# Kernel tuning notes

Hardware: AMD Instinct MI355X
Metric: run time of the kernel (lower is better)

## Reference

```python
import jax, jax.numpy as jnp
import numpy as np

B, S, C = 16, 720, 862      # batch, seq_len, enc_in
P = 24                      # highest_freq_period
PAD = 720                   # seq_len % P == 0 -> pad_len == seq_len (no padding branch taken)
LQ = PAD // P               # 30, per-branch subsequence length == conv channels
DM = 128                    # d_model (PECBlock hidden conv channels)
EL = 2                      # e_layers
PRED = 336                  # pred_len
EPS = 1e-5                  # RevIN eps


def setup_inputs() -> dict:
    key = jax.random.key(0)
    ks = jax.random.split(key, 6)
    x = jax.random.normal(ks[0], (B, S, C), jnp.float32)
    # per-layer, per-branch pointwise conv weights (kernel_size=1, no bias)
    W1 = jax.random.normal(ks[1], (EL, P, DM, LQ), jnp.float32) * 0.05   # conv1: LQ -> DM
    W2 = jax.random.normal(ks[2], (EL, P, LQ, DM), jnp.float32) * 0.05   # conv2: DM -> LQ
    proj_w = jax.random.normal(ks[3], (PRED, S), jnp.float32) * 0.02      # Linear(seq_len, pred_len)
    proj_b = jnp.zeros((PRED,), jnp.float32)
    rev_w = jnp.ones((C,), jnp.float32)    # RevIN affine weight
    rev_b = jnp.zeros((C,), jnp.float32)   # RevIN affine bias
    return dict(x=x, W1=W1, W2=W2, proj_w=proj_w, proj_b=proj_b, rev_w=rev_w, rev_b=rev_b)


def reference(x, W1, W2, proj_w, proj_b, rev_w, rev_b):
    # RevIN 'norm': stats over time dim (unbiased=False var), affine
    mean = jnp.mean(x, axis=1, keepdims=True)
    stdev = jnp.sqrt(jnp.var(x, axis=1, keepdims=True) + EPS)
    xn = (x - mean) / stdev * rev_w + rev_b

    # seq_len % P == 0 so pad_time_series is identity
    x_padded = xn
    # NOTE: original loop feeds x_padded into EVERY block (not chained),
    # so each iteration overwrites y; replicated faithfully.
    # Strided gather idx::P == reshape (B,C,LQ,P) and index last axis;
    # scatter reassembly y[:,:,idx::P]=... == reshape back from (B,C,LQ,P).
    xs = x_padded.transpose(0, 2, 1).reshape(B, C, LQ, P)  # (B,C,LQ,P)
    y = x_padded
    for l in range(EL):
        h = jax.nn.gelu(jnp.einsum('pdq,bcqp->pbdc', W1[l], xs), approximate=False)  # (P,B,DM,C)
        ys = jnp.einsum('pqd,pbdc->bcqp', W2[l], h)                                  # (B,C,LQ,P)
        y = ys.reshape(B, C, PAD).transpose(0, 2, 1)                                 # (B,PAD,C)

    # PredictedProjection: Linear over time dim
    out = jnp.einsum('ps,bsc->bpc', proj_w, y[:, :S, :]) + proj_b[None, :, None]  # (B,PRED,C)

    # RevIN 'denorm'
    out = (out - rev_b) / (rev_w + EPS * EPS)
    out = out * stdev + mean
    return out
```

## Files before the change

### kernel.cpp

```cpp
#include <hip/hip_runtime.h>
#include <math.h>

typedef __attribute__((ext_vector_type(8))) short bf16x8;
typedef __attribute__((ext_vector_type(4))) short short4v;
typedef __attribute__((ext_vector_type(4))) float f32x4;

#define NB 16
#define NS 720
#define NC 862
#define NP 24
#define NQ 30
#define NDM 128
#define NPRED 336
#define BC (NB*NC)
#define SCH 10
#define SLEN 72
#define KP 768
#define PBASE (4*BC)
#define WOFF_F (24*BC)
#define NCOL (NB*NC)

__device__ __forceinline__ short f2bf(float f) {
    union { float f; unsigned u; } v; v.f = f;
    unsigned r = v.u + 0x7FFFu + ((v.u >> 16) & 1u);
    return (short)(r >> 16);
}

__device__ __forceinline__ float gelu_f(float h) {
    float hc = fminf(fmaxf(h, -8.f), 8.f);
    float z2 = hc * hc;
    float zz = hc * (0.79788456f + 0.035677408f * z2);
    float e  = __expf(-2.f * zz);
    return h * __builtin_amdgcn_rcpf(1.f + e);
}

__device__ __forceinline__ void gl_lds16(const void* g, void* l) {
    __builtin_amdgcn_global_load_lds(
        (const __attribute__((address_space(1))) unsigned int*)g,
        (__attribute__((address_space(3))) unsigned int*)l, 16, 0, 0);
}

__global__ __launch_bounds__(256) void stats_partial_k(const float* __restrict__ x,
                                                       float* __restrict__ ws) {
    int b = blockIdx.x, half = blockIdx.y, ch = blockIdx.z;
    int t = half * 256 + threadIdx.x;
    if (t >= NC / 2) return;
    const float2* xp = (const float2*)(x + ((size_t)b * NS + (size_t)ch * SLEN) * NC) + t;
    float2 s = {0.f, 0.f}, sq = {0.f, 0.f};
    #pragma unroll 4
    for (int i = 0; i < SLEN; ++i) {
        float2 v = xp[(size_t)i * (NC / 2)];
        s.x += v.x; s.y += v.y;
        sq.x += v.x * v.x; sq.y += v.y * v.y;
    }
    int idx = b * NC + t * 2;
    float* ps = ws + PBASE;
    *(float2*)&ps[(size_t)ch * BC + idx] = s;
    *(float2*)&ps[(size_t)(SCH + ch) * BC + idx] = sq;
}

__global__ __launch_bounds__(256) void stats_final_k(float* __restrict__ ws,
                                                     const float* __restrict__ revw,
                                                     const float* __restrict__ revb) {
    int idx = blockIdx.x * 256 + threadIdx.x;
    if (idx >= BC) return;
    const float* ps = ws + PBASE;
    float s = 0.f, sq = 0.f;
    #pragma unroll
    for (int ch = 0; ch < SCH; ++ch) {
        s  += ps[(size_t)ch * BC + idx];
        sq += ps[(size_t)(SCH + ch) * BC + idx];
    }
    int c = idx % NC;
    float mean  = s * (1.f / NS);
    float var   = sq * (1.f / NS) - mean * mean;
    float stdev = sqrtf(var + 1e-5f);
    float rstd  = 1.f / stdev;
    float aw = revw[c] * rstd;
    float u  = stdev / (revw[c] + 1e-10f);
    ws[idx]          = aw;
    ws[BC + idx]     = revb[c] - mean * aw;
    ws[2 * BC + idx] = u;
    ws[3 * BC + idx] = mean - revb[c] * u;
}

__global__ __launch_bounds__(256) void wprep_k(const float* __restrict__ W1,
                                               const float* __restrict__ W2,
                                               unsigned short* __restrict__ W1FF,
                                               unsigned short* __restrict__ W2FF) {
    int p = blockIdx.x, tid = threadIdx.x;
    const float* w1 = W1 + (size_t)(NP + p) * NDM * NQ;
    const float* w2 = W2 + (size_t)(NP + p) * NQ * NDM;
    #pragma unroll
    for (int pass = 0; pass < 2; ++pass) {
        int s = pass * 256 + tid;
        int l = s & 63, lr = l & 15, lg = l >> 4;
        {
            int dt = s >> 6;
            int d = dt * 16 + lr;
            bf16x8 v;
            #pragma unroll
            for (int j = 0; j < 8; ++j) {
                int q = 8 * lg + j;
                v[j] = f2bf(q < NQ ? w1[d * NQ + q] : 0.f);
            }
            ((bf16x8*)(W1FF + (size_t)p * 4096))[s] = v;
        }
        {
            int g = s >> 6, mi = g >> 2, ks = g & 3;
            int q = mi * 16 + lr, k = ks * 32 + 8 * lg;
            bf16x8 v;
            #pragma unroll
            for (int j = 0; j < 8; ++j)
                v[j] = f2bf(q < NQ ? w2[q * NDM + k + j] : 0.f);
            ((bf16x8*)(W2FF + (size_t)p * 4096))[s] = v;
        }
    }
}

__global__ __launch_bounds__(256) void pwprep_k(const float* __restrict__ pw,
                                                unsigned short* __restrict__ PWPF) {
    int t = blockIdx.x * 256 + threadIdx.x;
    if (t >= 24 * 24 * 64) return;
    int l = t & 63, ks = (t >> 6) % 24, st = t / (24 * 64);
    int lr = l & 15, lg = l >> 4;
    int m = st * 16 + lr;
    bf16x8 v;
    #pragma unroll
    for (int j = 0; j < 8; ++j) {
        int q = 8 * lg + j;
        v[j] = f2bf((m < NPRED && q < NQ) ? pw[(size_t)m * NS + q * NP + ks] : 0.f);
    }
    ((bf16x8*)PWPF)[t] = v;
}

__global__ __launch_bounds__(256) void branch_k(const float* __restrict__ x,
        const unsigned short* __restrict__ W1FF, const unsigned short* __restrict__ W2FF,
        const float* __restrict__ ws, unsigned short* __restrict__ y_t) {
    __shared__ __align__(16) short XsB[4 * 64 * 8];
    __shared__ __align__(16) short HB [16 * 64 * 8];
    int tid = threadIdx.x;
    int c0 = blockIdx.x * 64;
    int p  = blockIdx.y;
    int b  = blockIdx.z;

    {
        int c  = tid & 63, kb = tid >> 6;
        int cg = c0 + c;
        bool cv = cg < NC;
        int ce = cv ? cg : NC - 1;
        float aw = ws[b * NC + ce];
        float bw = ws[BC + b * NC + ce];
        const float* xb = x + ((size_t)b * NS + p) * NC + ce;
        bf16x8 v;
        #pragma unroll
        for (int j = 0; j < 8; ++j) {
            int q = kb * 8 + j;
            float val = (q < NQ && cv) ? xb[(size_t)q * NP * NC] * aw + bw : 0.f;
            v[j] = f2bf(val);
        }
        *(bf16x8*)&XsB[(size_t)(kb * 64 + (c ^ kb)) * 8] = v;
    }

    int w = tid >> 6, l = tid & 63, lr = l & 15, lg = l >> 4;
    f32x4 zf = {0.f, 0.f, 0.f, 0.f};
    const bf16x8* w1p = (const bf16x8*)(W1FF + (size_t)p * 4096);
    const bf16x8* w2p = (const bf16x8*)(W2FF + (size_t)p * 4096);
    bf16x8 a0 = w1p[(2 * w) * 64 + l];
    bf16x8 a1 = w1p[(2 * w + 1) * 64 + l];

    __syncthreads();

    f32x4 hc[2][4];
    #pragma unroll
    for (int ni = 0; ni < 4; ++ni) {
        bf16x8 bfr = *(const bf16x8*)&XsB[(size_t)(lg * 64 + ((ni * 16 + lr) ^ lg)) * 8];
        hc[0][ni] = __builtin_amdgcn_mfma_f32_16x16x32_bf16(a0, bfr, zf, 0, 0, 0);
        hc[1][ni] = __builtin_amdgcn_mfma_f32_16x16x32_bf16(a1, bfr, zf, 0, 0, 0);
    }
    #pragma unroll
    for (int mi2 = 0; mi2 < 2; ++mi2) {
        int d0 = (2 * w + mi2) * 16 + 4 * lg;
        int kb = d0 >> 3, sub = d0 & 7;
        #pragma unroll
        for (int ni = 0; ni < 4; ++ni) {
            short4v v;
            #pragma unroll
            for (int r = 0; r < 4; ++r)
                v[r] = f2bf(gelu_f(hc[mi2][ni][r]));
            int col = ni * 16 + lr;
            *(short4v*)&HB[(size_t)(kb * 64 + (col ^ kb)) * 8 + sub] = v;
        }
    }
    __syncthreads();

    f32x4 yacc[2] = {zf, zf};
    #pragma unroll
    for (int ks = 0; ks < 4; ++ks) {
        int kb = ks * 4 + lg;
        bf16x8 hfr = *(const bf16x8*)&HB[(size_t)(kb * 64 + ((w * 16 + lr) ^ kb)) * 8];
        #pragma unroll
        for (int mi = 0; mi < 2; ++mi) {
            bf16x8 w2f = w2p[(mi * 4 + ks) * 64 + l];
            yacc[mi] = __builtin_amdgcn_mfma_f32_16x16x32_bf16(w2f, hfr, yacc[mi], 0, 0, 0);
        }
    }
    int cg2 = c0 + w * 16 + lr;
    if (cg2 < NC) {
        unsigned short* base = y_t + ((size_t)(b * NC + cg2)) * KP + p * 32;
        #pragma unroll
        for (int mi = 0; mi < 2; ++mi) {
            int q0 = mi * 16 + 4 * lg;
            short4v v;
            #pragma unroll
            for (int r = 0; r < 4; ++r)
                v[r] = (q0 + r < NQ) ? f2bf(yacc[mi][r]) : (short)0;
            *(short4v*)(base + q0) = v;
        }
    }
}

__global__ __launch_bounds__(256, 3) void proj_k(const unsigned short* __restrict__ PWPF,
        const float* __restrict__ pb, const float* __restrict__ ws,
        const unsigned short* __restrict__ y_t, float* __restrict__ out) {
    __shared__ __align__(16) short L[2][16 * 512];
    int tid = threadIdx.x;
    int w = tid >> 6, l = tid & 63, lr = l & 15, lg = l >> 4;
    int wm = w >> 1, wn = w & 1;
    int n0 = blockIdx.x * 128, m0 = blockIdx.y * 128;
    f32x4 zf = {0.f, 0.f, 0.f, 0.f};
    f32x4 acc[4][4];
    #pragma unroll
    for (int mi = 0; mi < 4; ++mi)
        #pragma unroll
        for (int nj = 0; nj < 4; ++nj) acc[mi][nj] = zf;

    int cB0 = n0 + w * 16 + lr;        if (cB0 > NCOL - 1) cB0 = NCOL - 1;
    int cB1 = n0 + (w + 4) * 16 + lr;  if (cB1 > NCOL - 1) cB1 = NCOL - 1;
    const unsigned short* sA0 = PWPF + ((size_t)(m0 / 16 + w) * 24) * 512 + (size_t)l * 8;
    const unsigned short* sA1 = PWPF + ((size_t)(m0 / 16 + w + 4) * 24) * 512 + (size_t)l * 8;
    const unsigned short* sB0 = y_t + (size_t)cB0 * KP + lg * 8;
    const unsigned short* sB1 = y_t + (size_t)cB1 * KP + lg * 8;

#define STAGE(BUF, KS) do {                                          \
        gl_lds16(sA0 + (size_t)(KS) * 512, &L[BUF][(w) * 512]);      \
        gl_lds16(sA1 + (size_t)(KS) * 512, &L[BUF][(w + 4) * 512]);  \
        gl_lds16(sB0 + (size_t)(KS) * 32,  &L[BUF][(8 + w) * 512]);  \
        gl_lds16(sB1 + (size_t)(KS) * 32,  &L[BUF][(12 + w) * 512]); \
    } while (0)

    STAGE(0, 0);
    __syncthreads();
    int cur = 0;
    for (int ks = 0; ks < 24; ++ks) {
        if (ks + 1 < 24) STAGE(cur ^ 1, ks + 1);
        const short* Lc = L[cur];
        bf16x8 bfr[4];
        #pragma unroll
        for (int nj = 0; nj < 4; ++nj)
            bfr[nj] = *(const bf16x8*)&Lc[(8 + wn * 4 + nj) * 512 + l * 8];
        #pragma unroll
        for (int mi = 0; mi < 4; ++mi) {
            bf16x8 a = *(const bf16x8*)&Lc[(wm * 4 + mi) * 512 + l * 8];
            #pragma unroll
            for (int nj = 0; nj < 4; ++nj)
                acc[mi][nj] = __builtin_amdgcn_mfma_f32_16x16x32_bf16(a, bfr[nj], acc[mi][nj], 0, 0, 0);
        }
        __syncthreads();
        cur ^= 1;
    }
#undef STAGE

    #pragma unroll
    for (int mi = 0; mi < 4; ++mi) {
        #pragma unroll
        for (int r = 0; r < 4; ++r) {
            int pr = m0 + wm * 64 + mi * 16 + 4 * lg + r;
            if (pr >= NPRED) continue;
            float bias = pb[pr];
            #pragma unroll
            for (int nj = 0; nj < 4; ++nj) {
                int cg = n0 + (wn * 4 + nj) * 16 + lr;
                if (cg >= NCOL) continue;
                int bb = cg / NC;
                int cc = cg - bb * NC;
                out[((size_t)bb * NPRED + pr) * NC + cc] =
                    (acc[mi][nj][r] + bias) * ws[2 * BC + cg] + ws[3 * BC + cg];
            }
        }
    }
}

extern "C" void kernel_launch(void* const* d_in, const int* in_sizes, int n_in,
                              void* d_out, int out_size, void* d_ws, size_t ws_size,
                              hipStream_t stream) {
    const float* x   = (const float*)d_in[0];
    const float* W1  = (const float*)d_in[1];
    const float* W2  = (const float*)d_in[2];
    const float* pw  = (const float*)d_in[3];
    const float* pb  = (const float*)d_in[4];
    const float* rw  = (const float*)d_in[5];
    const float* rb  = (const float*)d_in[6];
    float* out = (float*)d_out;
    float* ws  = (float*)d_ws;
    unsigned short* W1FF = (unsigned short*)(ws + WOFF_F);
    unsigned short* W2FF = W1FF + NP * 4096;
    unsigned short* PWPF = W2FF + NP * 4096;
    unsigned short* y_t  = PWPF + 24 * 24 * 64 * 8;

    stats_partial_k<<<dim3(NB, 2, SCH), 256, 0, stream>>>(x, ws);
    wprep_k<<<dim3(NP), 256, 0, stream>>>(W1, W2, W1FF, W2FF);
    pwprep_k<<<dim3((24 * 24 * 64 + 255) / 256), 256, 0, stream>>>(pw, PWPF);
    stats_final_k<<<dim3((BC + 255) / 256), 256, 0, stream>>>(ws, rw, rb);
    branch_k<<<dim3(14, NP, NB), 256, 0, stream>>>(x, W1FF, W2FF, ws, y_t);
    proj_k<<<dim3((NCOL + 127) / 128, 3), 256, 0, stream>>>(PWPF, pb, ws, y_t, out);
}
```

Before: 85.62 us.

## Loop branch kernel over six periods with prefetch; triple-buffer projection GEMM

The branch kernel now processes six period branches per block. It double-buffers the normalized input tile in LDS and prefetches the next branch's x values into registers while computing the current one, which cuts the grid size and overlaps global loads with MFMA work. The projection GEMM moves to 64-row M tiles with a three-stage LDS ring and explicit vmcnt waits plus a single barrier per k-step. That deepens load prefetch and doubles the block count, at the cost of less A reuse per block and more register pressure.

```diff
diff --git a/kernel.cpp b/kernel.cpp
--- a/kernel.cpp
+++ b/kernel.cpp
@@ -134,88 +134,110 @@
     ((bf16x8*)PWPF)[t] = v;
 }
 
-__global__ __launch_bounds__(256) void branch_k(const float* __restrict__ x,
+__global__ __launch_bounds__(256, 3) void branch_k(const float* __restrict__ x,
         const unsigned short* __restrict__ W1FF, const unsigned short* __restrict__ W2FF,
         const float* __restrict__ ws, unsigned short* __restrict__ y_t) {
-    __shared__ __align__(16) short XsB[4 * 64 * 8];
+    __shared__ __align__(16) short XsB[2][4 * 64 * 8];
     __shared__ __align__(16) short HB [16 * 64 * 8];
     int tid = threadIdx.x;
     int c0 = blockIdx.x * 64;
-    int p  = blockIdx.y;
+    int pg = blockIdx.y * 6;
     int b  = blockIdx.z;
 
-    {
-        int c  = tid & 63, kb = tid >> 6;
-        int cg = c0 + c;
-        bool cv = cg < NC;
-        int ce = cv ? cg : NC - 1;
-        float aw = ws[b * NC + ce];
-        float bw = ws[BC + b * NC + ce];
-        const float* xb = x + ((size_t)b * NS + p) * NC + ce;
-        bf16x8 v;
-        #pragma unroll
-        for (int j = 0; j < 8; ++j) {
-            int q = kb * 8 + j;
-            float val = (q < NQ && cv) ? xb[(size_t)q * NP * NC] * aw + bw : 0.f;
-            v[j] = f2bf(val);
-        }
-        *(bf16x8*)&XsB[(size_t)(kb * 64 + (c ^ kb)) * 8] = v;
-    }
+    int cS = tid & 63, kbS = tid >> 6;
+    int cgS = c0 + cS;
+    bool cv = cgS < NC;
+    int ce = cv ? cgS : NC - 1;
+    float aw = ws[b * NC + ce];
+    float bw = ws[BC + b * NC + ce];
+    const float* xb = x + (size_t)b * NS * NC + ce;
 
     int w = tid >> 6, l = tid & 63, lr = l & 15, lg = l >> 4;
     f32x4 zf = {0.f, 0.f, 0.f, 0.f};
-    const bf16x8* w1p = (const bf16x8*)(W1FF + (size_t)p * 4096);
-    const bf16x8* w2p = (const bf16x8*)(W2FF + (size_t)p * 4096);
-    bf16x8 a0 = w1p[(2 * w) * 64 + l];
-    bf16x8 a1 = w1p[(2 * w + 1) * 64 + l];
-
-    __syncthreads();
-
-    f32x4 hc[2][4];
-    #pragma unroll
-    for (int ni = 0; ni < 4; ++ni) {
-        bf16x8 bfr = *(const bf16x8*)&XsB[(size_t)(lg * 64 + ((ni * 16 + lr) ^ lg)) * 8];
-        hc[0][ni] = __builtin_amdgcn_mfma_f32_16x16x32_bf16(a0, bfr, zf, 0, 0, 0);
-        hc[1][ni] = __builtin_amdgcn_mfma_f32_16x16x32_bf16(a1, bfr, zf, 0, 0, 0);
-    }
-    #pragma unroll
-    for (int mi2 = 0; mi2 < 2; ++mi2) {
-        int d0 = (2 * w + mi2) * 16 + 4 * lg;
-        int kb = d0 >> 3, sub = d0 & 7;
+
+    {
+        bf16x8 v;
+        #pragma unroll
+        for (int j = 0; j < 8; ++j) {
+            int q = kbS * 8 + j;
+            float val = (q < NQ && cv) ? xb[(size_t)(q * NP + pg) * NC] * aw + bw : 0.f;
+            v[j] = f2bf(val);
+        }
+        *(bf16x8*)&XsB[0][(size_t)(kbS * 64 + (cS ^ kbS)) * 8] = v;
+    }
+
+    int cg2 = c0 + w * 16 + lr;
+    for (int pp = 0; pp < 6; ++pp) {
+        int p = pg + pp;
+        const bf16x8* w1p = (const bf16x8*)(W1FF + (size_t)p * 4096);
+        const bf16x8* w2p = (const bf16x8*)(W2FF + (size_t)p * 4096);
+        __syncthreads();
+
+        float xn[8];
+        if (pp < 5) {
+            #pragma unroll
+            for (int j = 0; j < 8; ++j) {
+                int q = kbS * 8 + j;
+                xn[j] = (q < NQ && cv) ? xb[(size_t)(q * NP + p + 1) * NC] * aw + bw : 0.f;
+            }
+        }
+        bf16x8 w2f[8];
+        #pragma unroll
+        for (int g = 0; g < 8; ++g) w2f[g] = w2p[g * 64 + l];
+
+        bf16x8 a0 = w1p[(2 * w) * 64 + l];
+        bf16x8 a1 = w1p[(2 * w + 1) * 64 + l];
+        f32x4 hc[2][4];
         #pragma unroll
         for (int ni = 0; ni < 4; ++ni) {
-            short4v v;
-            #pragma unroll
-            for (int r = 0; r < 4; ++r)
-                v[r] = f2bf(gelu_f(hc[mi2][ni][r]));
-            int col = ni * 16 + lr;
-            *(short4v*)&HB[(size_t)(kb * 64 + (col ^ kb)) * 8 + sub] = v;
-        }
-    }
-    __syncthreads();
-
-    f32x4 yacc[2] = {zf, zf};
-    #pragma unroll
-    for (int ks = 0; ks < 4; ++ks) {
-        int kb = ks * 4 + lg;
-        bf16x8 hfr = *(const bf16x8*)&HB[(size_t)(kb * 64 + ((w * 16 + lr) ^ kb)) * 8];
-        #pragma unroll
-        for (int mi = 0; mi < 2; ++mi) {
-            bf16x8 w2f = w2p[(mi * 4 + ks) * 64 + l];
-            yacc[mi] = __builtin_amdgcn_mfma_f32_16x16x32_bf16(w2f, hfr, yacc[mi], 0, 0, 0);
-        }
-    }
-    int cg2 = c0 + w * 16 + lr;
-    if (cg2 < NC) {
-        unsigned short* base = y_t + ((size_t)(b * NC + cg2)) * KP + p * 32;
-        #pragma unroll
-        for (int mi = 0; mi < 2; ++mi) {
-            int q0 = mi * 16 + 4 * lg;
-            short4v v;
-            #pragma unroll
-            for (int r = 0; r < 4; ++r)
-                v[r] = (q0 + r < NQ) ? f2bf(yacc[mi][r]) : (short)0;
-            *(short4v*)(base + q0) = v;
+            bf16x8 bfr = *(const bf16x8*)&XsB[pp & 1]
+                             [(size_t)(lg * 64 + ((ni * 16 + lr) ^ lg)) * 8];
+            hc[0][ni] = __builtin_amdgcn_mfma_f32_16x16x32_bf16(a0, bfr, zf, 0, 0, 0);
+            hc[1][ni] = __builtin_amdgcn_mfma_f32_16x16x32_bf16(a1, bfr, zf, 0, 0, 0);
+        }
+        #pragma unroll
+        for (int mi2 = 0; mi2 < 2; ++mi2) {
+            int d0 = (2 * w + mi2) * 16 + 4 * lg;
+            int kb = d0 >> 3, sub = d0 & 7;
+            #pragma unroll
+            for (int ni = 0; ni < 4; ++ni) {
+                short4v v;
+                #pragma unroll
+                for (int r = 0; r < 4; ++r)
+                    v[r] = f2bf(gelu_f(hc[mi2][ni][r]));
+                int col = ni * 16 + lr;
+                *(short4v*)&HB[(size_t)(kb * 64 + (col ^ kb)) * 8 + sub] = v;
+            }
+        }
+        __syncthreads();
+
+        f32x4 yacc[2] = {zf, zf};
+        #pragma unroll
+        for (int ks = 0; ks < 4; ++ks) {
+            int kb = ks * 4 + lg;
+            bf16x8 hfr = *(const bf16x8*)&HB[(size_t)(kb * 64 + ((w * 16 + lr) ^ kb)) * 8];
+            #pragma unroll
+            for (int mi = 0; mi < 2; ++mi)
+                yacc[mi] = __builtin_amdgcn_mfma_f32_16x16x32_bf16(w2f[mi * 4 + ks], hfr,
+                                                                  yacc[mi], 0, 0, 0);
+        }
+        if (cg2 < NC) {
+            unsigned short* base = y_t + ((size_t)(b * NC + cg2)) * KP + p * 32;
+            #pragma unroll
+            for (int mi = 0; mi < 2; ++mi) {
+                int q0 = mi * 16 + 4 * lg;
+                short4v v;
+                #pragma unroll
+                for (int r = 0; r < 4; ++r)
+                    v[r] = (q0 + r < NQ) ? f2bf(yacc[mi][r]) : (short)0;
+                *(short4v*)(base + q0) = v;
+            }
+        }
+        if (pp < 5) {
+            bf16x8 v;
+            #pragma unroll
+            for (int j = 0; j < 8; ++j) v[j] = f2bf(xn[j]);
+            *(bf16x8*)&XsB[(pp + 1) & 1][(size_t)(kbS * 64 + (cS ^ kbS)) * 8] = v;
         }
     }
 }
@@ -223,51 +245,42 @@
 __global__ __launch_bounds__(256, 3) void proj_k(const unsigned short* __restrict__ PWPF,
         const float* __restrict__ pb, const float* __restrict__ ws,
         const unsigned short* __restrict__ y_t, float* __restrict__ out) {
-    __shared__ __align__(16) short L[2][16 * 512];
+    __shared__ __align__(16) short L[3][12 * 512];
     int tid = threadIdx.x;
     int w = tid >> 6, l = tid & 63, lr = l & 15, lg = l >> 4;
-    int wm = w >> 1, wn = w & 1;
-    int n0 = blockIdx.x * 128, m0 = blockIdx.y * 128;
+    int n0 = blockIdx.x * 128, m0 = blockIdx.y * 64;
     f32x4 zf = {0.f, 0.f, 0.f, 0.f};
-    f32x4 acc[4][4];
-    #pragma unroll
-    for (int mi = 0; mi < 4; ++mi)
-        #pragma unroll
-        for (int nj = 0; nj < 4; ++nj) acc[mi][nj] = zf;
-
-    int cB0 = n0 + w * 16 + lr;        if (cB0 > NCOL - 1) cB0 = NCOL - 1;
-    int cB1 = n0 + (w + 4) * 16 + lr;  if (cB1 > NCOL - 1) cB1 = NCOL - 1;
-    const unsigned short* sA0 = PWPF + ((size_t)(m0 / 16 + w) * 24) * 512 + (size_t)l * 8;
-    const unsigned short* sA1 = PWPF + ((size_t)(m0 / 16 + w + 4) * 24) * 512 + (size_t)l * 8;
+    f32x4 acc[4][2];
+    #pragma unroll
+    for (int mi = 0; mi < 4; ++mi) { acc[mi][0] = zf; acc[mi][1] = zf; }
+
+    int cB0 = n0 + (2 * w) * 16 + lr;      if (cB0 > NCOL - 1) cB0 = NCOL - 1;
+    int cB1 = n0 + (2 * w + 1) * 16 + lr;  if (cB1 > NCOL - 1) cB1 = NCOL - 1;
+    const unsigned short* sA  = PWPF + ((size_t)(m0 / 16 + w) * 24) * 512 + (size_t)l * 8;
     const unsigned short* sB0 = y_t + (size_t)cB0 * KP + lg * 8;
     const unsigned short* sB1 = y_t + (size_t)cB1 * KP + lg * 8;
 
 #define STAGE(BUF, KS) do {                                          \
-        gl_lds16(sA0 + (size_t)(KS) * 512, &L[BUF][(w) * 512]);      \
-        gl_lds16(sA1 + (size_t)(KS) * 512, &L[BUF][(w + 4) * 512]);  \
-        gl_lds16(sB0 + (size_t)(KS) * 32,  &L[BUF][(8 + w) * 512]);  \
-        gl_lds16(sB1 + (size_t)(KS) * 32,  &L[BUF][(12 + w) * 512]); \
-    } while (0)
+        gl_lds16(sA  + (size_t)(KS) * 512, &L[BUF][w * 512]);        \
+        gl_lds16(sB0 + (size_t)(KS) * 32,  &L[BUF][(4 + 2 * w) * 512]); \
+        gl_lds16(sB1 + (size_t)(KS) * 32,  &L[BUF][(5 + 2 * w) * 512]); } while (0)
 
     STAGE(0, 0);
-    __syncthreads();
-    int cur = 0;
+    STAGE(1, 1);
+    #pragma unroll
     for (int ks = 0; ks < 24; ++ks) {
-        if (ks + 1 < 24) STAGE(cur ^ 1, ks + 1);
-        const short* Lc = L[cur];
-        bf16x8 bfr[4];
-        #pragma unroll
-        for (int nj = 0; nj < 4; ++nj)
-            bfr[nj] = *(const bf16x8*)&Lc[(8 + wn * 4 + nj) * 512 + l * 8];
+        if (ks < 23) asm volatile("s_waitcnt vmcnt(3)\n\ts_barrier" ::: "memory");
+        else         asm volatile("s_waitcnt vmcnt(0)\n\ts_barrier" ::: "memory");
+        const short* Lc = L[ks % 3];
+        bf16x8 b0 = *(const bf16x8*)&Lc[(4 + 2 * w) * 512 + l * 8];
+        bf16x8 b1 = *(const bf16x8*)&Lc[(5 + 2 * w) * 512 + l * 8];
         #pragma unroll
         for (int mi = 0; mi < 4; ++mi) {
-            bf16x8 a = *(const bf16x8*)&Lc[(wm * 4 + mi) * 512 + l * 8];
-            #pragma unroll
-            for (int nj = 0; nj < 4; ++nj)
-                acc[mi][nj] = __builtin_amdgcn_mfma_f32_16x16x32_bf16(a, bfr[nj], acc[mi][nj], 0, 0, 0);
-        }
-        __syncthreads();
-        cur ^= 1;
+            bf16x8 a = *(const bf16x8*)&Lc[mi * 512 + l * 8];
+            acc[mi][0] = __builtin_amdgcn_mfma_f32_16x16x32_bf16(a, b0, acc[mi][0], 0, 0, 0);
+            acc[mi][1] = __builtin_amdgcn_mfma_f32_16x16x32_bf16(a, b1, acc[mi][1], 0, 0, 0);
+        }
+        if (ks + 2 < 24) STAGE((ks + 2) % 3, ks + 2);
     }
 #undef STAGE
 
@@ -275,12 +288,12 @@
     for (int mi = 0; mi < 4; ++mi) {
         #pragma unroll
         for (int r = 0; r < 4; ++r) {
-            int pr = m0 + wm * 64 + mi * 16 + 4 * lg + r;
+            int pr = m0 + mi * 16 + 4 * lg + r;
             if (pr >= NPRED) continue;
             float bias = pb[pr];
             #pragma unroll
-            for (int nj = 0; nj < 4; ++nj) {
-                int cg = n0 + (wn * 4 + nj) * 16 + lr;
+            for (int nj = 0; nj < 2; ++nj) {
+                int cg = n0 + (2 * w + nj) * 16 + lr;
                 if (cg >= NCOL) continue;
                 int bb = cg / NC;
                 int cc = cg - bb * NC;
@@ -312,6 +325,6 @@
     wprep_k<<<dim3(NP), 256, 0, stream>>>(W1, W2, W1FF, W2FF);
     pwprep_k<<<dim3((24 * 24 * 64 + 255) / 256), 256, 0, stream>>>(pw, PWPF);
     stats_final_k<<<dim3((BC + 255) / 256), 256, 0, stream>>>(ws, rw, rb);
-    branch_k<<<dim3(14, NP, NB), 256, 0, stream>>>(x, W1FF, W2FF, ws, y_t);
-    proj_k<<<dim3((NCOL + 127) / 128, 3), 256, 0, stream>>>(PWPF, pb, ws, y_t, out);
-}
+    branch_k<<<dim3(14, 4, NB), 256, 0, stream>>>(x, W1FF, W2FF, ws, y_t);
+    proj_k<<<dim3((NCOL + 127) / 128, 6), 256, 0, stream>>>(PWPF, pb, ws, y_t, out);
+}
```

Result: slower. 91.34 us (+6.7%).
